# Kernel tuning notes

Measured on AMD Instinct MI355X. Metric: run time of the kernel, lower is better.

## Reference

```python
import jax, jax.numpy as jnp
import numpy as np

B, S, D = 4, 2048, 1024
EPS = 1e-5


def setup_inputs() -> dict:
    key = jax.random.key(0)
    ks = jax.random.split(key, 8)
    s = 1.0 / np.sqrt(D)
    return {
        "x": jax.random.normal(ks[0], (B, S, D), dtype=jnp.float32),
        "Wq": jax.random.normal(ks[1], (D, D), dtype=jnp.float32) * s,
        "Wk": jax.random.normal(ks[2], (D, D), dtype=jnp.float32) * s,
        "Wv": jax.random.normal(ks[3], (D, D), dtype=jnp.float32) * s,
        "W1": jax.random.normal(ks[4], (D, D), dtype=jnp.float32) * s,
        "b1": jnp.zeros((D,), dtype=jnp.float32),
        "W2": jax.random.normal(ks[5], (D, D), dtype=jnp.float32) * s,
        "b2": jnp.zeros((D,), dtype=jnp.float32),
        "gamma": jnp.ones((D,), dtype=jnp.float32),
        "beta": jnp.zeros((D,), dtype=jnp.float32),
    }


def _layer_norm(x, gamma, beta):
    mu = jnp.mean(x, axis=-1, keepdims=True)
    var = jnp.mean(jnp.square(x - mu), axis=-1, keepdims=True)
    return (x - mu) * jax.lax.rsqrt(var + EPS) * gamma + beta


def reference(x, Wq, Wk, Wv, W1, b1, W2, b2, gamma, beta):
    seq_len, d = x.shape[1], x.shape[2]
    # torch Linear: y = x @ W.T
    Q = jnp.einsum('bsd,ed->bse', x, Wq)
    K = jnp.einsum('bsd,ed->bse', x, Wk)
    V = jnp.einsum('bsd,ed,->bse', x, Wv, jnp.float32(1.0)) if False else jnp.einsum('bsd,ed->bse', x, Wv)
    scores = jnp.einsum('bqd,bkd->bqk', Q, K) / jnp.sqrt(jnp.float32(d))
    causal = jnp.tril(jnp.ones((seq_len, seq_len), dtype=bool))  # [S,S]
    scores = jnp.where(causal[None, :, :], scores, -jnp.inf)
    attn = jax.nn.softmax(scores, axis=-1)
    attn_out = jnp.einsum('bqk,bkd->bqd', attn, V)
    # dropout is identity at eval
    h = _layer_norm(x + attn_out, gamma, beta)
    ff = jnp.einsum('bsd,ed->bse', jax.nn.relu(jnp.einsum('bsd,ed->bse', h, W1) + b1), W2) + b2
    out = _layer_norm(h + ff, gamma, beta)
    return out
```

## Files before the change

### kernel.cpp

```cpp
#include <hip/hip_runtime.h>
#include <math.h>
#include <cstdint>
#include <cstddef>

#define DI __device__ __forceinline__

typedef __bf16 bf16x8 __attribute__((ext_vector_type(8)));
typedef float f32x4 __attribute__((ext_vector_type(4)));
typedef unsigned short ushort8 __attribute__((ext_vector_type(8)));

static constexpr int kB = 4, kS = 2048, kD = 1024;
static constexpr int kM = kB * kS;
static constexpr float kScale = 0.03125f;
static constexpr float kEps = 1e-5f;

DI unsigned short f2bf(float f) {
  unsigned u = __float_as_uint(f);
  u += 0x7FFFu + ((u >> 16) & 1u);
  return (unsigned short)(u >> 16);
}
DI float bf2f(unsigned short h) {
  return __uint_as_float(((unsigned)h) << 16);
}

DI void gld_lds16(const void* g, void* l) {
  __builtin_amdgcn_global_load_lds(
      (__attribute__((address_space(1))) void*)(void*)g,
      (__attribute__((address_space(3))) void*)l, 16, 0, 0);
}

#define SBAR() __builtin_amdgcn_sched_barrier(0)
#define FULLBAR() do { SBAR(); __builtin_amdgcn_s_barrier(); SBAR(); } while (0)

__global__ __launch_bounds__(256) void k_cast_all(
    const float* __restrict__ x, const float* __restrict__ Wq,
    const float* __restrict__ Wk, const float* __restrict__ Wv,
    const float* __restrict__ W1, const float* __restrict__ W2,
    unsigned short* __restrict__ xb, unsigned short* __restrict__ Wqkb,
    unsigned short* __restrict__ Wvb, unsigned short* __restrict__ W1b,
    unsigned short* __restrict__ W2b) {
  const int i = blockIdx.x * 256 + threadIdx.x;
  const int X4 = kM * kD / 4;
  const int W4 = kD * kD / 4;
  const float* src;
  unsigned short* dst;
  int j;
  if (i < X4) { src = x; dst = xb; j = i; }
  else if (i < X4 + W4)     { src = Wq; dst = Wqkb;          j = i - X4; }
  else if (i < X4 + 2 * W4) { src = Wk; dst = Wqkb + 4 * W4; j = i - X4 - W4; }
  else if (i < X4 + 3 * W4) { src = Wv; dst = Wvb;           j = i - X4 - 2 * W4; }
  else if (i < X4 + 4 * W4) { src = W1; dst = W1b;           j = i - X4 - 3 * W4; }
  else                      { src = W2; dst = W2b;           j = i - X4 - 4 * W4; }
  float4 v = ((const float4*)src)[j];
  ushort4 o;
  o.x = f2bf(v.x); o.y = f2bf(v.y); o.z = f2bf(v.z); o.w = f2bf(v.w);
  ((ushort4*)dst)[j] = o;
}

template <int NF, int OUT_BF16, int RELU>
__global__ __launch_bounds__(512, 2) void k_gemm8p(
    const unsigned short* __restrict__ A, const unsigned short* __restrict__ B,
    void* __restrict__ Cv, const float* __restrict__ bias,
    int M, int N, int K, int lda, int ldb, int ldc,
    long sA, long sB, long sC, int cColOff) {
  constexpr int BN = NF * 64;
  constexpr int LB = BN / 128;
  constexpr int VM = 2 + 2 * LB;
  constexpr int AH = 256 * 32;
  constexpr int BH = BN * 32;

  int lin = blockIdx.x + gridDim.x * blockIdx.y;
  const int nblk = gridDim.x * gridDim.y;
  if ((nblk & 7) == 0)
    lin = (lin & 7) * (nblk >> 3) + (lin >> 3);
  const int bm = (lin / gridDim.x) * 256;
  const int bn = (lin % gridDim.x) * BN;
  A += (long)blockIdx.z * sA;
  B += (long)blockIdx.z * sB;

  const int tid = threadIdx.x;
  const int lane = tid & 63;
  const int wm = (tid >> 6) >> 2;
  const int wn = (tid >> 6) & 3;
  const int fm = lane & 15;
  const int fq = lane >> 4;

  __shared__ __align__(16) unsigned short Asm[2 * 2 * AH];
  __shared__ __align__(16) unsigned short Bsm[2 * 2 * BH];

  long aoff[2];
#pragma unroll
  for (int i = 0; i < 2; ++i) {
    const int ci = i * 512 + tid;
    const int row = ci >> 2;
    const int g = (ci & 3) ^ ((row >> 1) & 3);
    aoff[i] = (long)(bm + row) * lda + g * 8;
  }
  long boff[LB];
#pragma unroll
  for (int i = 0; i < LB; ++i) {
    const int ci = i * 512 + tid;
    const int row = ci >> 2;
    const int g = (ci & 3) ^ ((row >> 1) & 3);
    boff[i] = (long)(bn + row) * ldb + g * 8;
  }

  const int NT = K >> 6;

  auto stA = [&](int d, int kh, int t) {
    const unsigned short* s = A + t * 64 + kh * 32;
    unsigned short* dst = Asm + (d * 2 + kh) * AH;
#pragma unroll
    for (int i = 0; i < 2; ++i)
      gld_lds16(s + aoff[i], dst + (i * 512 + tid) * 8);
  };
  auto stB = [&](int d, int kh, int t) {
    const unsigned short* s = B + t * 64 + kh * 32;
    unsigned short* dst = Bsm + (d * 2 + kh) * BH;
#pragma unroll
    for (int i = 0; i < LB; ++i)
      gld_lds16(s + boff[i], dst + (i * 512 + tid) * 8);
  };

  const int slotoff = (fq ^ ((fm >> 1) & 3)) * 8;
  const unsigned short* aRd = Asm + (wm * 128 + fm) * 32 + slotoff;
  const unsigned short* bRd = Bsm + (wn * (NF * 16) + fm) * 32 + slotoff;

  f32x4 acc[8][NF];
#pragma unroll
  for (int m = 0; m < 8; ++m)
#pragma unroll
    for (int n = 0; n < NF; ++n) acc[m][n] = (f32x4){0.f, 0.f, 0.f, 0.f};

  stB(0, 0, 0); stA(0, 0, 0); stB(0, 1, 0); stA(0, 1, 0);
  if (NT > 1) { stB(1, 0, 1); stA(1, 0, 1); stB(1, 1, 1); }
  SBAR();
  asm volatile("s_waitcnt vmcnt(%0)" :: "i"(VM) : "memory");
  __builtin_amdgcn_s_barrier();
  SBAR();

  bf16x8 af[4], bfr[NF];

  for (int t = 0; t < NT; ++t) {
    const int d = t & 1;
    const unsigned short* aB0 = aRd + d * (2 * AH);
    const unsigned short* bB0 = bRd + d * (2 * BH);
    const unsigned short* aB1 = aB0 + AH;
    const unsigned short* bB1 = bB0 + BH;

#pragma unroll
    for (int m = 0; m < 4; ++m) af[m] = *(const bf16x8*)(aB0 + m * 512);
#pragma unroll
    for (int n = 0; n < NF; ++n) bfr[n] = *(const bf16x8*)(bB0 + n * 512);
    if (t + 1 < NT) stA(d ^ 1, 1, t + 1);
    FULLBAR();
    __builtin_amdgcn_s_setprio(1);
#pragma unroll
    for (int m = 0; m < 4; ++m)
#pragma unroll
      for (int n = 0; n < NF; ++n)
        acc[m][n] = __builtin_amdgcn_mfma_f32_16x16x32_bf16(af[m], bfr[n], acc[m][n], 0, 0, 0);
    __builtin_amdgcn_s_setprio(0);
    FULLBAR();

#pragma unroll
    for (int m = 0; m < 4; ++m) af[m] = *(const bf16x8*)(aB0 + (4 + m) * 512);
    if (t + 2 < NT) stB(d, 0, t + 2);
    FULLBAR();
    __builtin_amdgcn_s_setprio(1);
#pragma unroll
    for (int m = 0; m < 4; ++m)
#pragma unroll
      for (int n = 0; n < NF; ++n)
        acc[4 + m][n] = __builtin_amdgcn_mfma_f32_16x16x32_bf16(af[m], bfr[n], acc[4 + m][n], 0, 0, 0);
    __builtin_amdgcn_s_setprio(0);
    FULLBAR();

#pragma unroll
    for (int m = 0; m < 4; ++m) af[m] = *(const bf16x8*)(aB1 + m * 512);
#pragma unroll
    for (int n = 0; n < NF; ++n) bfr[n] = *(const bf16x8*)(bB1 + n * 512);
    if (t + 2 < NT) stA(d, 0, t + 2);
    FULLBAR();
    __builtin_amdgcn_s_setprio(1);
#pragma unroll
    for (int m = 0; m < 4; ++m)
#pragma unroll
      for (int n = 0; n < NF; ++n)
        acc[m][n] = __builtin_amdgcn_mfma_f32_16x16x32_bf16(af[m], bfr[n], acc[m][n], 0, 0, 0);
    __builtin_amdgcn_s_setprio(0);
    FULLBAR();

#pragma unroll
    for (int m = 0; m < 4; ++m) af[m] = *(const bf16x8*)(aB1 + (4 + m) * 512);
    if (t + 2 < NT) stB(d, 1, t + 2);
    SBAR();
    if (t < NT - 2)
      asm volatile("s_waitcnt vmcnt(%0)" :: "i"(VM) : "memory");
    else
      asm volatile("s_waitcnt vmcnt(0)" ::: "memory");
    __builtin_amdgcn_s_barrier();
    SBAR();
    __builtin_amdgcn_s_setprio(1);
#pragma unroll
    for (int m = 0; m < 4; ++m)
#pragma unroll
      for (int n = 0; n < NF; ++n)
        acc[4 + m][n] = __builtin_amdgcn_mfma_f32_16x16x32_bf16(af[m], bfr[n], acc[4 + m][n], 0, 0, 0);
    __builtin_amdgcn_s_setprio(0);
    FULLBAR();
  }

  const long cb = (long)blockIdx.z * sC;
  float bv[NF];
#pragma unroll
  for (int n = 0; n < NF; ++n)
    bv[n] = bias ? bias[bn + wn * (NF * 16) + n * 16 + fm] : 0.f;
#pragma unroll
  for (int m = 0; m < 8; ++m) {
#pragma unroll
    for (int r = 0; r < 4; ++r) {
      const int row = bm + wm * 128 + m * 16 + fq * 4 + r;
#pragma unroll
      for (int n = 0; n < NF; ++n) {
        const int col = cColOff + bn + wn * (NF * 16) + n * 16 + fm;
        float v = acc[m][n][r] + bv[n];
        if (RELU) v = fmaxf(v, 0.f);
        if (OUT_BF16)
          ((unsigned short*)Cv)[cb + (long)row * ldc + col] = f2bf(v);
        else
          ((float*)Cv)[cb + (long)row * ldc + col] = v;
      }
    }
  }
}

template <int OUT_BF16, int RELU, int CAUSAL>
__global__ __launch_bounds__(256, 2) void k_gemm_nt(
    const unsigned short* __restrict__ A, const unsigned short* __restrict__ B,
    void* __restrict__ Cv, const float* __restrict__ bias,
    int M, int N, int K, int lda, int ldb, int ldc,
    long sA, long sB, long sC) {
  int bm, bn;
  {
    int lin = blockIdx.x + gridDim.x * blockIdx.y;
    const int nblk = gridDim.x * gridDim.y;
    if ((nblk & 7) == 0)
      lin = (lin & 7) * (nblk >> 3) + (lin >> 3);
    if (CAUSAL == 1) {
      const int t = lin;
      int r = (int)floorf((sqrtf(8.f * (float)t + 1.f) - 1.f) * 0.5f);
      while ((r + 1) * (r + 2) / 2 <= t) ++r;
      while (r * (r + 1) / 2 > t) --r;
      bm = r * 128;
      bn = (t - r * (r + 1) / 2) * 128;
    } else {
      bm = (lin / gridDim.x) * 128;
      bn = (lin % gridDim.x) * 128;
    }
  }
  A += (long)blockIdx.z * sA;
  B += (long)blockIdx.z * sB;

  const int tid = threadIdx.x;
  const int lane = tid & 63;
  const int wm = ((tid >> 6) >> 1) * 64;
  const int wn = ((tid >> 6) & 1) * 64;

  __shared__ __align__(16) unsigned short Asm[128 * 64];
  __shared__ __align__(16) unsigned short Bsm[128 * 64];

  f32x4 acc[4][4];
#pragma unroll
  for (int i = 0; i < 4; ++i)
#pragma unroll
    for (int j = 0; j < 4; ++j) acc[i][j] = (f32x4){0.f, 0.f, 0.f, 0.f};

  const int r_row = tid >> 3;
  const int dst_k = (tid & 7) * 8;
  const int src_k = ((tid & 7) ^ ((tid >> 3) & 7)) * 8;
  const int fm = lane & 15;
  const int fq = lane >> 4;

  for (int k0 = 0; k0 < K; k0 += 64) {
#pragma unroll
    for (int i = 0; i < 4; ++i) {
      const int row = i * 32 + r_row;
      gld_lds16(A + (long)(bm + row) * lda + (k0 + src_k), Asm + row * 64 + dst_k);
      gld_lds16(B + (long)(bn + row) * ldb + (k0 + src_k), Bsm + row * 64 + dst_k);
    }
    __syncthreads();
#pragma unroll
    for (int kk = 0; kk < 2; ++kk) {
      bf16x8 af[4], bfr[4];
#pragma unroll
      for (int i = 0; i < 4; ++i) {
        const int pa = ((kk * 4 + fq) ^ (fm & 7)) * 8;
        af[i]  = *(const bf16x8*)(Asm + (wm + i * 16 + fm) * 64 + pa);
        bfr[i] = *(const bf16x8*)(Bsm + (wn + i * 16 + fm) * 64 + pa);
      }
#pragma unroll
      for (int i = 0; i < 4; ++i)
#pragma unroll
        for (int j = 0; j < 4; ++j)
          acc[i][j] = __builtin_amdgcn_mfma_f32_16x16x32_bf16(af[i], bfr[j], acc[i][j], 0, 0, 0);
    }
    __syncthreads();
  }

  const long cb = (long)blockIdx.z * sC;
#pragma unroll
  for (int i = 0; i < 4; ++i) {
#pragma unroll
    for (int j = 0; j < 4; ++j) {
      const int col = bn + wn + j * 16 + fm;
      const float bv = bias ? bias[col] : 0.f;
#pragma unroll
      for (int r = 0; r < 4; ++r) {
        const int row = bm + wm + i * 16 + fq * 4 + r;
        float v = acc[i][j][r] + bv;
        if (RELU) v = fmaxf(v, 0.f);
        if (OUT_BF16)
          ((unsigned short*)Cv)[cb + (long)row * ldc + col] = f2bf(v);
        else
          ((float*)Cv)[cb + (long)row * ldc + col] = v;
      }
    }
  }
}

__global__ __launch_bounds__(256, 2) void k_attn_pv(
    const unsigned short* __restrict__ P, const unsigned short* __restrict__ Vt,
    unsigned short* __restrict__ O) {
  const int r = blockIdx.x;
  const int q = blockIdx.y + 16 * blockIdx.z;
  const int lx = q & 7;
  const int pq = r + 8 * (q >> 3);
  const int pair = pq & 15;
  const int zz = pq >> 4;

  const int bn = lx * 128;
  const int bm_hi = (31 - pair) * 64;
  const int bm_lo = pair * 64;
  const int Khi = bm_hi + 64;
  const int Klo = bm_lo + 64;
  P  += (long)zz * kS * kS;
  Vt += (long)zz * kD * kS;
  O  += (long)zz * kS * kD;

  const int tid = threadIdx.x;
  const int lane = tid & 63;
  const int wn = (tid >> 6) * 32;

  __shared__ __align__(16) unsigned short Ah[64 * 64];
  __shared__ __align__(16) unsigned short Al[64 * 64];
  __shared__ __align__(16) unsigned short Bs[128 * 64];

  f32x4 ah[4][2], al[4][2];
#pragma unroll
  for (int i = 0; i < 4; ++i)
#pragma unroll
    for (int j = 0; j < 2; ++j) {
      ah[i][j] = (f32x4){0.f, 0.f, 0.f, 0.f};
      al[i][j] = (f32x4){0.f, 0.f, 0.f, 0.f};
    }

  const int r_row = tid >> 3;
  const int dst_k = (tid & 7) * 8;
  const int src_k = ((tid & 7) ^ ((tid >> 3) & 7)) * 8;
  const int fm = lane & 15;
  const int fq = lane >> 4;

  for (int k0 = 0; k0 < Khi; k0 += 64) {
    const bool lo = (k0 < Klo);
#pragma unroll
    for (int i = 0; i < 2; ++i) {
      const int row = i * 32 + r_row;
      gld_lds16(P + (long)(bm_hi + row) * kS + (k0 + src_k), Ah + row * 64 + dst_k);
      if (lo)
        gld_lds16(P + (long)(bm_lo + row) * kS + (k0 + src_k), Al + row * 64 + dst_k);
    }
#pragma unroll
    for (int i = 0; i < 4; ++i) {
      const int row = i * 32 + r_row;
      gld_lds16(Vt + (long)(bn + row) * kS + (k0 + src_k), Bs + row * 64 + dst_k);
    }
    __syncthreads();
#pragma unroll
    for (int kk = 0; kk < 2; ++kk) {
      bf16x8 afh[4], afl[4], bfr[2];
#pragma unroll
      for (int i = 0; i < 4; ++i) {
        const int ra = i * 16 + fm;
        const int pa = ((kk * 4 + fq) ^ (ra & 7)) * 8;
        afh[i] = *(const bf16x8*)(Ah + ra * 64 + pa);
        afl[i] = *(const bf16x8*)(Al + ra * 64 + pa);
      }
#pragma unroll
      for (int j = 0; j < 2; ++j) {
        const int rb = wn + j * 16 + fm;
        const int pb = ((kk * 4 + fq) ^ (rb & 7)) * 8;
        bfr[j] = *(const bf16x8*)(Bs + rb * 64 + pb);
      }
#pragma unroll
      for (int i = 0; i < 4; ++i)
#pragma unroll
        for (int j = 0; j < 2; ++j)
          ah[i][j] = __builtin_amdgcn_mfma_f32_16x16x32_bf16(afh[i], bfr[j], ah[i][j], 0, 0, 0);
      if (lo) {
#pragma unroll
        for (int i = 0; i < 4; ++i)
#pragma unroll
          for (int j = 0; j < 2; ++j)
            al[i][j] = __builtin_amdgcn_mfma_f32_16x16x32_bf16(afl[i], bfr[j], al[i][j], 0, 0, 0);
      }
    }
    __syncthreads();
  }

#pragma unroll
  for (int i = 0; i < 4; ++i) {
#pragma unroll
    for (int j = 0; j < 2; ++j) {
      const int col = bn + wn + j * 16 + fm;
#pragma unroll
      for (int r2 = 0; r2 < 4; ++r2) {
        const int rr = i * 16 + fq * 4 + r2;
        O[(long)(bm_hi + rr) * kD + col] = f2bf(ah[i][j][r2]);
        O[(long)(bm_lo + rr) * kD + col] = f2bf(al[i][j][r2]);
      }
    }
  }
}

DI float wsum(float v) {
  v += __shfl_xor(v, 32, 64);
  v += __shfl_xor(v, 16, 64);
  v += __shfl_xor(v, 8, 64);
  v += __shfl_xor(v, 4, 64);
  v += __shfl_xor(v, 2, 64);
  v += __shfl_xor(v, 1, 64);
  return v;
}
DI float wmax(float v) {
  v = fmaxf(v, __shfl_xor(v, 32, 64));
  v = fmaxf(v, __shfl_xor(v, 16, 64));
  v = fmaxf(v, __shfl_xor(v, 8, 64));
  v = fmaxf(v, __shfl_xor(v, 4, 64));
  v = fmaxf(v, __shfl_xor(v, 2, 64));
  v = fmaxf(v, __shfl_xor(v, 1, 64));
  return v;
}

__global__ __launch_bounds__(256) void k_softmax_causal(
    const unsigned short* __restrict__ S, unsigned short* __restrict__ P) {
  const int row = blockIdx.x;
  const int q = row & (kS - 1);
  const int lim = (q & ~127) + 128;
  const unsigned short* Srow = S + (long)row * kS;
  unsigned short* Prow = P + (long)row * kS;
  const int tid = threadIdx.x;
  const int k0 = tid * 8;
  __shared__ float red[4];

  const ushort8 s = *(const ushort8*)(Srow + k0);
  float v[8];
  float mx = -INFINITY;
#pragma unroll
  for (int j = 0; j < 8; ++j) {
    const float xv = (k0 + j <= q) ? bf2f(s[j]) * kScale : -INFINITY;
    v[j] = xv;
    mx = fmaxf(mx, xv);
  }
  mx = wmax(mx);
  if ((tid & 63) == 0) red[tid >> 6] = mx;
  __syncthreads();
  mx = fmaxf(fmaxf(red[0], red[1]), fmaxf(red[2], red[3]));
  __syncthreads();

  float sum = 0.f;
#pragma unroll
  for (int j = 0; j < 8; ++j) {
    const float e = (v[j] > -INFINITY) ? __expf(v[j] - mx) : 0.f;
    v[j] = e;
    sum += e;
  }
  sum = wsum(sum);
  if ((tid & 63) == 0) red[tid >> 6] = sum;
  __syncthreads();
  sum = red[0] + red[1] + red[2] + red[3];
  const float inv = 1.f / sum;
  if (k0 < lim) {
    ushort8 o;
#pragma unroll
    for (int j = 0; j < 8; ++j) o[j] = f2bf(v[j] * inv);
    *(ushort8*)(Prow + k0) = o;
  }
}

template <int X_BF16, int OUT_FP32>
__global__ __launch_bounds__(256) void k_residual_ln(
    const void* __restrict__ Xv, const unsigned short* __restrict__ Yb,
    const float* __restrict__ gamma, const float* __restrict__ beta,
    float* __restrict__ Out, unsigned short* __restrict__ OutB) {
  const long base = (long)blockIdx.x * kD;
  const int tid = threadIdx.x;
  __shared__ float reds[4], redss[4];
  float v[4];
  float s = 0.f, ss2 = 0.f;
#pragma unroll
  for (int i = 0; i < 4; ++i) {
    const int k = tid + i * 256;
    const float xf = X_BF16 ? bf2f(((const unsigned short*)Xv)[base + k])
                            : ((const float*)Xv)[base + k];
    const float xv = xf + bf2f(Yb[base + k]);
    v[i] = xv;
    s += xv;
    ss2 += xv * xv;
  }
  s = wsum(s);
  ss2 = wsum(ss2);
  if ((tid & 63) == 0) { reds[tid >> 6] = s; redss[tid >> 6] = ss2; }
  __syncthreads();
  s = reds[0] + reds[1] + reds[2] + reds[3];
  ss2 = redss[0] + redss[1] + redss[2] + redss[3];
  const float mu = s * (1.f / kD);
  float var = ss2 * (1.f / kD) - mu * mu;
  var = fmaxf(var, 0.f);
  const float rstd = rsqrtf(var + kEps);
#pragma unroll
  for (int i = 0; i < 4; ++i) {
    const int k = tid + i * 256;
    const float y = (v[i] - mu) * rstd * gamma[k] + beta[k];
    if (OUT_FP32) Out[base + k] = y;
    else          OutB[base + k] = f2bf(y);
  }
}

extern "C" void kernel_launch(void* const* d_in, const int* in_sizes, int n_in,
                              void* d_out, int out_size, void* d_ws, size_t ws_size,
                              hipStream_t stream) {
  (void)in_sizes; (void)n_in; (void)out_size; (void)ws_size;
  const float* x     = (const float*)d_in[0];
  const float* Wq    = (const float*)d_in[1];
  const float* Wk    = (const float*)d_in[2];
  const float* Wv    = (const float*)d_in[3];
  const float* W1    = (const float*)d_in[4];
  const float* b1    = (const float*)d_in[5];
  const float* W2    = (const float*)d_in[6];
  const float* b2    = (const float*)d_in[7];
  const float* gamma = (const float*)d_in[8];
  const float* beta  = (const float*)d_in[9];
  float* out = (float*)d_out;

  char* base = (char*)d_ws;
  size_t off = 0;
  auto alloc = [&](size_t bytes) -> void* {
    void* p = base + off;
    off = (off + bytes + 255) & ~(size_t)255;
    return p;
  };

  unsigned short* xb     = (unsigned short*)alloc((size_t)kM * kD * 2);
  unsigned short* Wqkb   = (unsigned short*)alloc((size_t)2 * kD * kD * 2);
  unsigned short* Wvb    = (unsigned short*)alloc((size_t)kD * kD * 2);
  unsigned short* W1b    = (unsigned short*)alloc((size_t)kD * kD * 2);
  unsigned short* W2b    = (unsigned short*)alloc((size_t)kD * kD * 2);
  unsigned short* QKb    = (unsigned short*)alloc((size_t)kM * 2 * kD * 2);
  unsigned short* Vt     = (unsigned short*)alloc((size_t)kM * kD * 2);
  unsigned short* Sb     = (unsigned short*)alloc((size_t)kB * kS * kS * 2);
  unsigned short* Pb     = (unsigned short*)alloc((size_t)kB * kS * kS * 2);
  unsigned short* attn_b = (unsigned short*)alloc((size_t)kM * kD * 2);
  unsigned short* ff_b = attn_b;
  unsigned short* hb   = Sb;
  unsigned short* mid  = Pb;

  dim3 blk(256);
  dim3 blk8(512);

  {
    const int n4 = (kM * kD + 5 * kD * kD) / 4;
    k_cast_all<<<n4 / 256, blk, 0, stream>>>(x, Wq, Wk, Wv, W1, W2,
                                             xb, Wqkb, Wvb, W1b, W2b);
  }

  k_gemm_nt<1, 0, 0><<<dim3(2 * kD / 128, kM / 128, 1), blk, 0, stream>>>(
      xb, Wqkb, QKb, nullptr, kM, 2 * kD, kD, kD, kD, 2 * kD, 0, 0, 0);

  k_gemm8p<2, 1, 0><<<dim3(kS / 128, kD / 256, kB), blk8, 0, stream>>>(
      Wvb, xb, Vt, nullptr, kD, kS, kD, kD, kD, kS,
      0, (long)kS * kD, (long)kD * kS, 0);

  k_gemm_nt<1, 0, 1><<<dim3(136, 1, kB), blk, 0, stream>>>(
      QKb, QKb + kD, Sb, nullptr, kS, kS, kD, 2 * kD, 2 * kD, kS,
      (long)kS * 2 * kD, (long)kS * 2 * kD, (long)kS * kS);

  k_softmax_causal<<<kM, blk, 0, stream>>>(Sb, Pb);

  k_attn_pv<<<dim3(8, 16, kB), blk, 0, stream>>>(Pb, Vt, attn_b);

  k_residual_ln<0, 0><<<kM, blk, 0, stream>>>(x, attn_b, gamma, beta,
                                              nullptr, hb);

  k_gemm8p<2, 1, 1><<<dim3(kD / 128, kM / 256, 1), blk8, 0, stream>>>(
      hb, W1b, mid, b1, kM, kD, kD, kD, kD, kD, 0, 0, 0, 0);
  k_gemm8p<2, 1, 0><<<dim3(kD / 128, kM / 256, 1), blk8, 0, stream>>>(
      mid, W2b, ff_b, b2, kM, kD, kD, kD, kD, kD, 0, 0, 0, 0);

  k_residual_ln<1, 1><<<kM, blk, 0, stream>>>(hb, ff_b, gamma, beta,
                                              out, nullptr);
}
```

Measured before the change: 330.6 us.

## Fuse Q and K projections into a dual-output GEMM sharing the x tile

Replaces the generic 128x128 GEMM for the combined QK projection with a dedicated 512-thread kernel. Each block loads one x tile into shared memory and computes both the Q and K output tiles for the same columns, with half the waves on each, so A-tile loads are shared and x is read from global memory half as often. The kernel has a single LDS buffer with two barriers per k-step and no double buffering, and it writes the output as scattered scalar bf16 stores. Either could limit the gain from the reuse.

```diff
diff --git a/kernel.cpp b/kernel.cpp
--- a/kernel.cpp
+++ b/kernel.cpp
@@ -57,6 +57,87 @@
   ((ushort4*)dst)[j] = o;
 }
 
+__global__ __launch_bounds__(512, 2) void k_qk_dual(
+    const unsigned short* __restrict__ A, const unsigned short* __restrict__ B,
+    unsigned short* __restrict__ C) {
+  int lin = blockIdx.x + gridDim.x * blockIdx.y;
+  const int nblk = gridDim.x * gridDim.y;
+  lin = (lin & 7) * (nblk >> 3) + (lin >> 3);
+  const int bm = (lin >> 3) * 128;
+  const int bn = (lin & 7) * 128;
+
+  const int tid = threadIdx.x;
+  const int lane = tid & 63;
+  const int w = tid >> 6;
+  const int h = w >> 2;
+  const int s = w & 3;
+  const int wm = (s >> 1) * 64;
+  const int wn = (s & 1) * 64;
+  const int fm = lane & 15;
+  const int fq = lane >> 4;
+
+  __shared__ __align__(16) unsigned short Asm[128 * 64];
+  __shared__ __align__(16) unsigned short Bsm[2][128 * 64];
+
+  f32x4 acc[4][4];
+#pragma unroll
+  for (int i = 0; i < 4; ++i)
+#pragma unroll
+    for (int j = 0; j < 4; ++j) acc[i][j] = (f32x4){0.f, 0.f, 0.f, 0.f};
+
+  const int c = tid & 7;
+  int dst[2];
+  long asrc[2], bqsrc[2], bksrc[2];
+#pragma unroll
+  for (int i = 0; i < 2; ++i) {
+    const int row = (i * 512 + tid) >> 3;
+    const int g = c ^ (row & 7);
+    dst[i] = row * 64 + c * 8;
+    asrc[i]  = (long)(bm + row) * kD + g * 8;
+    bqsrc[i] = (long)(bn + row) * kD + g * 8;
+    bksrc[i] = (long)(kD + bn + row) * kD + g * 8;
+  }
+
+  for (int k0 = 0; k0 < kD; k0 += 64) {
+#pragma unroll
+    for (int i = 0; i < 2; ++i) {
+      gld_lds16(A + asrc[i] + k0, Asm + dst[i]);
+      gld_lds16(B + bqsrc[i] + k0, Bsm[0] + dst[i]);
+      gld_lds16(B + bksrc[i] + k0, Bsm[1] + dst[i]);
+    }
+    __syncthreads();
+#pragma unroll
+    for (int kk = 0; kk < 2; ++kk) {
+      bf16x8 af[4], bfr[4];
+#pragma unroll
+      for (int i = 0; i < 4; ++i) {
+        const int pa = ((kk * 4 + fq) ^ (fm & 7)) * 8;
+        af[i]  = *(const bf16x8*)(Asm + (wm + i * 16 + fm) * 64 + pa);
+        bfr[i] = *(const bf16x8*)(Bsm[h] + (wn + i * 16 + fm) * 64 + pa);
+      }
+#pragma unroll
+      for (int i = 0; i < 4; ++i)
+#pragma unroll
+        for (int j = 0; j < 4; ++j)
+          acc[i][j] = __builtin_amdgcn_mfma_f32_16x16x32_bf16(af[i], bfr[j], acc[i][j], 0, 0, 0);
+    }
+    __syncthreads();
+  }
+
+#pragma unroll
+  for (int i = 0; i < 4; ++i) {
+#pragma unroll
+    for (int j = 0; j < 4; ++j) {
+      const int col = h * kD + bn + wn + j * 16 + fm;
+#pragma unroll
+      for (int r = 0; r < 4; ++r) {
+        const int row = bm + wm + i * 16 + fq * 4 + r;
+        C[(long)row * (2 * kD) + col] = f2bf(acc[i][j][r]);
+      }
+    }
+  }
+}
+
 template <int NF, int OUT_BF16, int RELU>
 __global__ __launch_bounds__(512, 2) void k_gemm8p(
     const unsigned short* __restrict__ A, const unsigned short* __restrict__ B,
@@ -584,8 +665,7 @@
                                              xb, Wqkb, Wvb, W1b, W2b);
   }
 
-  k_gemm_nt<1, 0, 0><<<dim3(2 * kD / 128, kM / 128, 1), blk, 0, stream>>>(
-      xb, Wqkb, QKb, nullptr, kM, 2 * kD, kD, kD, kD, 2 * kD, 0, 0, 0);
+  k_qk_dual<<<dim3(8, kM / 128, 1), blk8, 0, stream>>>(xb, Wqkb, QKb);
 
   k_gemm8p<2, 1, 0><<<dim3(kS / 128, kD / 256, kB), blk8, 0, stream>>>(
       Wvb, xb, Vt, nullptr, kD, kS, kD, kD, kD, kS,
```

Result: no change. 325.4 us (-1.6%).
